# Performance work log

Measured on AMD Instinct MI355X. Metric: run time of the kernel, lower is better.

Reference implementation:

```python
import jax, jax.numpy as jnp
import numpy as np

EMB_DIM = 512
N_HEAD = 8
HEAD_DIM = EMB_DIM // N_HEAD
SEQ_LEN = 2048
BATCH = 4


def setup_inputs() -> dict:
    key = jax.random.key(0)
    k1, k2, k3 = jax.random.split(key, 3)
    emb = jax.random.normal(k1, (SEQ_LEN, BATCH, EMB_DIM), dtype=jnp.float32)
    # torch Linear weight layout: (out_features, in_features)
    W = jax.random.normal(k2, (3 * EMB_DIM, EMB_DIM), dtype=jnp.float32) * 0.02
    b = jax.random.normal(k3, (3 * EMB_DIM,), dtype=jnp.float32) * 0.02
    return {"emb": emb, "W": W, "b": b}


def reference(emb, W, b):
    L, B, E = emb.shape
    scaling = (E / N_HEAD) ** -0.5
    # qkv projection: (L, B, 3E)
    ft = jnp.einsum('lbe,oe->lbo', emb, W) + b
    # interleaved per-head qkv split, matching reshape(L, B*nh, -1).chunk(3, -1)
    ft = ft.reshape(L, B * N_HEAD, 3 * HEAD_DIM).transpose(1, 0, 2)  # (B*nh, L, 3*hd)
    q, k, v = jnp.split(ft, 3, axis=-1)  # each (B*nh, L, hd)
    # attention scores with value-based zero mask
    scores = jnp.einsum('bld,bmd->blm', q, k) * scaling  # (B*nh, L, L)
    mask = scores == 0
    scores = jnp.where(mask, -jnp.inf, scores)
    attn = jax.nn.softmax(scores, axis=-1)
    attn = jnp.where(mask, jnp.zeros((), attn.dtype), attn)
    out = jnp.einsum('blm,bmd->bld', attn, v)  # (B*nh, L, hd)
    out = out.transpose(1, 0, 2).reshape(L, B, E)
    return out
```

## Files before the change

kernel.cpp:

```cpp
#include <hip/hip_runtime.h>
#include <hip/hip_bf16.h>
#include <cstdint>
#include <math.h>


typedef __bf16 bf16x8 __attribute__((ext_vector_type(8)));
typedef float  f32x4  __attribute__((ext_vector_type(4)));
typedef float  f32x16 __attribute__((ext_vector_type(16)));
typedef unsigned int uint32x4 __attribute__((ext_vector_type(4)));

#define MFMA16(a, b, c) __builtin_amdgcn_mfma_f32_16x16x32_bf16(a, b, c, 0, 0, 0)
#define MFMA32(a, b, c) __builtin_amdgcn_mfma_f32_32x32x16_bf16(a, b, c, 0, 0, 0)

#define EXP2F(x) __builtin_amdgcn_exp2f(x)

#define QSCALE 0.18033688011112042f

enum {
  LSEQ = 2048,
  NBATCH = 4,
  EMB = 512,
  NHEAD = 8,
  HDIM = 64,
  NBH = NBATCH * NHEAD,
  MROWS = LSEQ * NBATCH,
  KDIM = EMB,
  NOUT = 3 * EMB
};

__device__ inline void gload_lds16(const void* g, void* l) {
  __builtin_amdgcn_global_load_lds(
      (__attribute__((address_space(1))) void*)(uintptr_t)g,
      (__attribute__((address_space(3))) void*)(uint32_t)(uintptr_t)l,
      16, 0, 0);
}

__device__ inline unsigned packbf(float a, float b) {
  unsigned short ua = __builtin_bit_cast(unsigned short, (__bf16)a);
  unsigned short ub = __builtin_bit_cast(unsigned short, (__bf16)b);
  return (unsigned)ua | ((unsigned)ub << 16);
}

__device__ inline bf16x8 frag_from(unsigned w0, unsigned w1, unsigned w2, unsigned w3) {
  uint32x4 v = {w0, w1, w2, w3};
  return __builtin_bit_cast(bf16x8, v);
}

__global__ __launch_bounds__(256) void cvt2_kernel(const float* __restrict__ a,
                                                   __bf16* __restrict__ oa, int na8,
                                                   const float* __restrict__ b,
                                                   __bf16* __restrict__ ob, int nb8) {
  int i = blockIdx.x * 256 + threadIdx.x;
  const float* in;
  __bf16* out;
  int idx;
  if (i < na8) {
    in = a; out = oa; idx = i;
  } else {
    idx = i - na8;
    if (idx >= nb8) return;
    in = b; out = ob;
  }
  const float4* p = (const float4*)in + (size_t)idx * 2;
  float4 x = p[0], y = p[1];
  bf16x8 o;
  o[0] = (__bf16)x.x; o[1] = (__bf16)x.y; o[2] = (__bf16)x.z; o[3] = (__bf16)x.w;
  o[4] = (__bf16)y.x; o[5] = (__bf16)y.y; o[6] = (__bf16)y.z; o[7] = (__bf16)y.w;
  *(bf16x8*)(out + (size_t)idx * 8) = o;
}

__global__ __launch_bounds__(256) void qkv_gemm_kernel(
    const __bf16* __restrict__ A, const __bf16* __restrict__ Bt,
    const float* __restrict__ bias,
    __bf16* __restrict__ Qh, __bf16* __restrict__ Kh, __bf16* __restrict__ Vth) {
  __shared__ __align__(16) __bf16 As[128 * 64];
  __shared__ __align__(16) __bf16 Bs[128 * 64];

  const int tid = threadIdx.x;
  const int wid = tid >> 6, lane = tid & 63;
  const int g = lane >> 4, lx = lane & 15;

  const int orig = blockIdx.x;
  const int xcd = orig & 7, rr = orig >> 3;
  const int mt_local = rr / 12;
  const int ntile = rr - mt_local * 12;
  const int mtile = xcd * 8 + mt_local;
  const int b = mtile >> 4;
  const int l0 = (mtile & 15) * 128;

  const int wm = (wid >> 1) * 64, wn = (wid & 1) * 64;
  const int lr = lane >> 3;
  const int lc = (lane & 7) * 8;

  f32x4 acc[4][4] = {};

  const int rowB0 = ntile * 128;

  for (int k0 = 0; k0 < KDIM; k0 += 64) {
#pragma unroll
    for (int i = 0; i < 4; ++i) {
      int chunk = wid * 4 + i;
      gload_lds16(A + ((size_t)(l0 + chunk * 8 + lr) * NBATCH + b) * KDIM + k0 + lc,
                  As + chunk * 512);
      gload_lds16(Bt + (size_t)(rowB0 + chunk * 8 + lr) * KDIM + k0 + lc,
                  Bs + chunk * 512);
    }
    __syncthreads();
#pragma unroll
    for (int kk = 0; kk < 2; ++kk) {
      bf16x8 af[4], bfr[4];
#pragma unroll
      for (int t = 0; t < 4; ++t)
        af[t] = *(const bf16x8*)&As[(wm + t * 16 + lx) * 64 + kk * 32 + g * 8];
#pragma unroll
      for (int t = 0; t < 4; ++t)
        bfr[t] = *(const bf16x8*)&Bs[(wn + t * 16 + lx) * 64 + kk * 32 + g * 8];
#pragma unroll
      for (int mi = 0; mi < 4; ++mi)
#pragma unroll
        for (int ni = 0; ni < 4; ++ni)
          acc[mi][ni] = MFMA16(af[mi], bfr[ni], acc[mi][ni]);
    }
    __syncthreads();
  }

#pragma unroll
  for (int ni = 0; ni < 4; ++ni) {
    int o = ntile * 128 + wn + ni * 16 + lx;
    float bv = bias[o];
    unsigned h = (unsigned)o / 192u;
    unsigned w = (unsigned)o - h * 192u;
    const size_t bh = (size_t)(b * NHEAD) + h;
#pragma unroll
    for (int mi = 0; mi < 4; ++mi) {
      const int l = l0 + wm + mi * 16 + g * 4;
      if (w < 64u) {
#pragma unroll
        for (int r = 0; r < 4; ++r)
          Qh[(bh * LSEQ + l + r) * HDIM + w] =
              (__bf16)((acc[mi][ni][r] + bv) * QSCALE);
      } else if (w < 128u) {
#pragma unroll
        for (int r = 0; r < 4; ++r)
          Kh[(bh * LSEQ + l + r) * HDIM + (w - 64u)] = (__bf16)(acc[mi][ni][r] + bv);
      } else {
        unsigned u0 = packbf(acc[mi][ni][0] + bv, acc[mi][ni][1] + bv);
        unsigned u1 = packbf(acc[mi][ni][2] + bv, acc[mi][ni][3] + bv);
        uint2 uv = make_uint2(u0, u1);
        *(uint2*)&Vth[(bh * HDIM + (w - 128u)) * LSEQ + l] = uv;
      }
    }
  }
}

__global__ __launch_bounds__(512, 2) void attn_kernel(const __bf16* __restrict__ Qh,
                                                      const __bf16* __restrict__ Kh,
                                                      const __bf16* __restrict__ Vth,
                                                      float* __restrict__ out) {
  __shared__ __align__(16) __bf16 Ks[4][64 * 64];
  __shared__ __align__(16) __bf16 Vs[4][64 * 64];

  const int flat = blockIdx.x;
  const int sw = (flat & 7) * 64 + (flat >> 3);
  const int bh = sw >> 4, qt = sw & 15;
  const int tid = threadIdx.x, wid = tid >> 6, lane = tid & 63;
  const int pair = wid >> 1, role = wid & 1;
  const int ql = lane & 31, hi = lane >> 5;
  const int rb = ql & 7;

  const __bf16* Kb = Kh + (size_t)bh * (LSEQ * HDIM);
  const __bf16* Vb = Vth + (size_t)bh * (HDIM * LSEQ);

  const __bf16* Qp =
      Qh + ((size_t)bh * LSEQ + qt * 128 + pair * 32 + ql) * HDIM + hi * 8;
  bf16x8 qf[4];
#pragma unroll
  for (int s = 0; s < 4; ++s) qf[s] = *(const bf16x8*)(Qp + s * 16);

  const int lr3 = lane >> 3;
  const int ch = (lane & 7) ^ lr3;

#define STAGE_T(tt)                                                        \
  {                                                                        \
    const int tn_ = (tt) & 31;                                             \
    const int b_ = tn_ & 3;                                                \
    gload_lds16(Kb + (size_t)(tn_ * 64 + wid * 8 + lr3) * HDIM + ch * 8,   \
                &Ks[b_][(wid * 8) * 64]);                                  \
    gload_lds16(Vb + (size_t)(wid * 8 + lr3) * LSEQ + tn_ * 64 + ch * 8,   \
                &Vs[b_][(wid * 8) * 64]);                                  \
  }

  int ko[4], vo[4];
#pragma unroll
  for (int fs = 0; fs < 4; ++fs)
    ko[fs] = (role * 32 + ql) * 64 + (((2 * fs + hi) ^ rb) << 3);
#pragma unroll
  for (int dt = 0; dt < 2; ++dt)
#pragma unroll
    for (int ks = 0; ks < 2; ++ks)
      vo[dt * 2 + ks] =
          (dt * 32 + ql) * 64 + (((role * 4 + 2 * ks + hi) ^ rb) << 3);

  f32x16 ot[2] = {};
  float lacc[8] = {};
  bf16x8 pfA[2], pfB[2];

#define HEAD                                           \
  asm volatile("s_waitcnt vmcnt(2)" ::: "memory");     \
  __builtin_amdgcn_s_barrier();                        \
  asm volatile("" ::: "memory");

#define FILL(pfX, s_)                                                        \
  {                                                                          \
    const int cur_ = (s_) & 3;                                               \
    const __bf16* kr_ = &Ks[cur_][0];                                        \
    bf16x8 k0 = *(const bf16x8*)(kr_ + ko[0]);                               \
    bf16x8 k1 = *(const bf16x8*)(kr_ + ko[1]);                               \
    bf16x8 k2 = *(const bf16x8*)(kr_ + ko[2]);                               \
    bf16x8 k3 = *(const bf16x8*)(kr_ + ko[3]);                               \
    f32x16 st_ = {};                                                         \
    __builtin_amdgcn_s_setprio(1);                                           \
    st_ = MFMA32(k0, qf[0], st_);                                            \
    st_ = MFMA32(k1, qf[1], st_);                                            \
    st_ = MFMA32(k2, qf[2], st_);                                            \
    st_ = MFMA32(k3, qf[3], st_);                                            \
    __builtin_amdgcn_s_setprio(0);                                           \
    _Pragma("unroll") for (int r = 0; r < 16; ++r) {                         \
      float e_ = EXP2F(st_[r]);                                              \
      st_[r] = e_;                                                           \
      lacc[r & 7] += e_;                                                     \
    }                                                                        \
    unsigned b0 = packbf(st_[0], st_[1]), b1 = packbf(st_[2], st_[3]);       \
    unsigned b2 = packbf(st_[4], st_[5]), b3 = packbf(st_[6], st_[7]);       \
    unsigned b4 = packbf(st_[8], st_[9]), b5 = packbf(st_[10], st_[11]);     \
    unsigned b6 = packbf(st_[12], st_[13]), b7 = packbf(st_[14], st_[15]);   \
    asm("v_permlane32_swap_b32 %0, %1" : "+v"(b0), "+v"(b2));                \
    asm("v_permlane32_swap_b32 %0, %1" : "+v"(b1), "+v"(b3));                \
    asm("v_permlane32_swap_b32 %0, %1" : "+v"(b4), "+v"(b6));                \
    asm("v_permlane32_swap_b32 %0, %1" : "+v"(b5), "+v"(b7));                \
    pfX[0] = frag_from(b0, b1, b2, b3);                                      \
    pfX[1] = frag_from(b4, b5, b6, b7);                                      \
  }

#define PVSTEP(pfX, bidx)                                  \
  {                                                        \
    const __bf16* vr_ = &Vs[bidx][0];                      \
    bf16x8 v0 = *(const bf16x8*)(vr_ + vo[0]);             \
    bf16x8 v1 = *(const bf16x8*)(vr_ + vo[1]);             \
    bf16x8 v2 = *(const bf16x8*)(vr_ + vo[2]);             \
    bf16x8 v3 = *(const bf16x8*)(vr_ + vo[3]);             \
    __builtin_amdgcn_s_setprio(1);                         \
    ot[0] = MFMA32(v0, pfX[0], ot[0]);                     \
    ot[0] = MFMA32(v1, pfX[1], ot[0]);                     \
    ot[1] = MFMA32(v2, pfX[0], ot[1]);                     \
    ot[1] = MFMA32(v3, pfX[1], ot[1]);                     \
    __builtin_amdgcn_s_setprio(0);                         \
  }

  STAGE_T(0);
  STAGE_T(1);

  HEAD;
  FILL(pfA, 0);
  STAGE_T(2);

  HEAD;
  FILL(pfB, 1);
  PVSTEP(pfA, 0);
  STAGE_T(3);

  for (int i = 0; i < 15; ++i) {
    const int s0 = 2 + 2 * i;
    HEAD;
    FILL(pfA, s0);
    PVSTEP(pfB, (s0 - 1) & 3);
    STAGE_T(s0 + 2);
    HEAD;
    FILL(pfB, s0 + 1);
    PVSTEP(pfA, s0 & 3);
    STAGE_T(s0 + 3);
  }
  PVSTEP(pfB, 3);

#undef STAGE_T
#undef HEAD
#undef FILL
#undef PVSTEP

  float ls = 0.f;
#pragma unroll
  for (int r = 0; r < 8; ++r) ls += lacc[r];
  ls += __shfl_xor(ls, 32);

  asm volatile("s_waitcnt vmcnt(0) lgkmcnt(0)" ::: "memory");
  __syncthreads();
  float* stash_ot = (float*)&Ks[0][0];
  float* stash_ls = (float*)&Vs[0][0];
  float* myo = stash_ot + (wid * 64 + lane) * 16;
  f32x16 give = role ? ot[0] : ot[1];
#pragma unroll
  for (int g4 = 0; g4 < 4; ++g4) {
    float4 v4 = make_float4(give[4 * g4 + 0], give[4 * g4 + 1],
                            give[4 * g4 + 2], give[4 * g4 + 3]);
    *(float4*)(myo + 4 * g4) = v4;
  }
  stash_ls[wid * 64 + lane] = ls;
  __syncthreads();

  const float* po = stash_ot + ((wid ^ 1) * 64 + lane) * 16;
  f32x16 mine = role ? ot[1] : ot[0];
#pragma unroll
  for (int r = 0; r < 16; ++r) mine[r] += po[r];
  const float lst = ls + stash_ls[(wid ^ 1) * 64 + lane];
  const float inv = 1.f / lst;

  const int lq = qt * 128 + pair * 32 + ql;
  float* ob = out + (size_t)lq * (NBATCH * EMB) + (bh >> 3) * EMB + (bh & 7) * HDIM;
#pragma unroll
  for (int g4 = 0; g4 < 4; ++g4) {
    float4 v4 = make_float4(mine[4 * g4 + 0] * inv, mine[4 * g4 + 1] * inv,
                            mine[4 * g4 + 2] * inv, mine[4 * g4 + 3] * inv);
    *(float4*)(ob + role * 32 + g4 * 8 + hi * 4) = v4;
  }
}

extern "C" void kernel_launch(void* const* d_in, const int* in_sizes, int n_in,
                              void* d_out, int out_size, void* d_ws, size_t ws_size,
                              hipStream_t stream) {
  const float* emb = (const float*)d_in[0];
  const float* W = (const float*)d_in[1];
  const float* bias = (const float*)d_in[2];
  float* out = (float*)d_out;

  char* ws = (char*)d_ws;
  __bf16* embh = (__bf16*)(ws);
  __bf16* Wh   = (__bf16*)(ws + 8388608);
  __bf16* Qh   = (__bf16*)(ws + 9961472);
  __bf16* Kh   = (__bf16*)(ws + 18350080);
  __bf16* Vth  = (__bf16*)(ws + 26738688);

  const int na8 = MROWS * KDIM / 8;
  const int nb8 = NOUT * KDIM / 8;
  cvt2_kernel<<<dim3((na8 + nb8 + 255) / 256), dim3(256), 0, stream>>>(
      emb, embh, na8, W, Wh, nb8);
  qkv_gemm_kernel<<<dim3(768), dim3(256), 0, stream>>>(
      embh, Wh, bias, Qh, Kh, Vth);
  attn_kernel<<<dim3(NBH * (LSEQ / 128)), dim3(512), 0, stream>>>(Qh, Kh, Vth, out);
}
```

Before: 88.91 us.

## Double-buffer QKV GEMM LDS tiles and XOR-swizzle shared memory layout

The QKV projection GEMM now uses two LDS buffers, issuing the global-to-LDS loads for the next K slice before computing on the current one, so load latency overlaps with MFMA work. The LDS layout also gets an XOR swizzle on the 16-byte chunk index, applied to both the global-load destination and the fragment reads, to cut bank conflicts. LDS use doubles to 64KB per block, which may lower occupancy. The GEMM is one part of a larger pipeline that includes attention.

```diff
diff --git a/kernel.cpp b/kernel.cpp
--- a/kernel.cpp
+++ b/kernel.cpp
@@ -73,8 +73,8 @@
     const __bf16* __restrict__ A, const __bf16* __restrict__ Bt,
     const float* __restrict__ bias,
     __bf16* __restrict__ Qh, __bf16* __restrict__ Kh, __bf16* __restrict__ Vth) {
-  __shared__ __align__(16) __bf16 As[128 * 64];
-  __shared__ __align__(16) __bf16 Bs[128 * 64];
+  __shared__ __align__(16) __bf16 As[2][128 * 64];
+  __shared__ __align__(16) __bf16 Bs[2][128 * 64];
 
   const int tid = threadIdx.x;
   const int wid = tid >> 6, lane = tid & 63;
@@ -90,31 +90,42 @@
 
   const int wm = (wid >> 1) * 64, wn = (wid & 1) * 64;
   const int lr = lane >> 3;
-  const int lc = (lane & 7) * 8;
+  const int ch = (lane & 7) ^ lr;
+
+  const int rowB0 = ntile * 128;
+
+#define GSTAGE(bufi, ks)                                                          \
+  {                                                                               \
+    _Pragma("unroll") for (int i = 0; i < 4; ++i) {                               \
+      const int chunk = wid * 4 + i;                                              \
+      gload_lds16(A + ((size_t)(l0 + chunk * 8 + lr) * NBATCH + b) * KDIM +       \
+                      (ks) * 64 + ch * 8,                                         \
+                  &As[bufi][chunk * 512]);                                        \
+      gload_lds16(Bt + (size_t)(rowB0 + chunk * 8 + lr) * KDIM + (ks) * 64 +      \
+                      ch * 8,                                                     \
+                  &Bs[bufi][chunk * 512]);                                        \
+    }                                                                             \
+  }
 
   f32x4 acc[4][4] = {};
 
-  const int rowB0 = ntile * 128;
-
-  for (int k0 = 0; k0 < KDIM; k0 += 64) {
-#pragma unroll
-    for (int i = 0; i < 4; ++i) {
-      int chunk = wid * 4 + i;
-      gload_lds16(A + ((size_t)(l0 + chunk * 8 + lr) * NBATCH + b) * KDIM + k0 + lc,
-                  As + chunk * 512);
-      gload_lds16(Bt + (size_t)(rowB0 + chunk * 8 + lr) * KDIM + k0 + lc,
-                  Bs + chunk * 512);
-    }
-    __syncthreads();
+  GSTAGE(0, 0);
+  __syncthreads();
+
+  for (int k = 0; k < 8; ++k) {
+    const int cur = k & 1;
+    if (k < 7) GSTAGE(cur ^ 1, k + 1);
 #pragma unroll
     for (int kk = 0; kk < 2; ++kk) {
       bf16x8 af[4], bfr[4];
 #pragma unroll
       for (int t = 0; t < 4; ++t)
-        af[t] = *(const bf16x8*)&As[(wm + t * 16 + lx) * 64 + kk * 32 + g * 8];
+        af[t] = *(const bf16x8*)&As[cur][(wm + t * 16 + lx) * 64 +
+                                         (((kk * 4 + g) ^ (lx & 7)) << 3)];
 #pragma unroll
       for (int t = 0; t < 4; ++t)
-        bfr[t] = *(const bf16x8*)&Bs[(wn + t * 16 + lx) * 64 + kk * 32 + g * 8];
+        bfr[t] = *(const bf16x8*)&Bs[cur][(wn + t * 16 + lx) * 64 +
+                                          (((kk * 4 + g) ^ (lx & 7)) << 3)];
 #pragma unroll
       for (int mi = 0; mi < 4; ++mi)
 #pragma unroll
@@ -123,6 +134,7 @@
     }
     __syncthreads();
   }
+#undef GSTAGE
 
 #pragma unroll
   for (int ni = 0; ni < 4; ++ni) {
```

Result: faster. 80.58 us (-9.4%).
